# Performance work log

Measured on AMD Instinct MI355X. Metric: run time of the kernel, lower is better.

The kernel has to match this reference:

```python
import jax, jax.numpy as jnp
import numpy as np
from jax import lax

RADIUS = 3
ITERATION = 6
KSIZE = 2 * RADIUS + 1


def _make_kernels(r):
    # Build the 8 directional side-window box kernels, order: L,R,U,D,NW,NE,SW,SE
    k = 2 * r + 1
    f = np.ones((k, k), np.float32)
    L = f.copy(); L[:, r + 1:] = 0
    R = f.copy(); R[:, :r] = 0
    U = f.copy(); U[r + 1:, :] = 0
    D = f.copy(); D[:r, :] = 0
    NW = U.copy(); NW[:, r + 1:] = 0
    NE = U.copy(); NE[:, :r] = 0
    SW = D.copy(); SW[:, r + 1:] = 0
    SE = D.copy(); SE[:, :r] = 0
    n_half = (r + 1) * k          # normalizer for half windows
    n_quarter = (r + 1) ** 2      # normalizer for quarter windows
    ks = np.stack([L / n_half, R / n_half, U / n_half, D / n_half,
                   NW / n_quarter, NE / n_quarter, SW / n_quarter, SE / n_quarter])
    return jnp.asarray(ks[:, None, :, :])  # (8,1,k,k) OIHW


def setup_inputs() -> dict:
    key = jax.random.key(0)
    k1, k2 = jax.random.split(key)
    im = jax.random.normal(k1, (4, 3, 512, 512), dtype=jnp.float32)
    pert = jax.random.normal(k2, (4, 3, 512, 512), dtype=jnp.float32)
    return {"im": im, "pert": pert}


def reference(im, pert):
    b, c, h, w = im.shape
    W = _make_kernels(RADIUS)

    def conv8(x):  # (N,1,h,w) -> (N,8,h,w), SAME padding of radius
        return lax.conv_general_dilated(
            x, W, window_strides=(1, 1),
            padding=[(RADIUS, RADIUS), (RADIUS, RADIUS)],
            dimension_numbers=("NCHW", "OIHW", "NCHW"))

    # channels are processed independently with identical kernels -> fold c into batch
    im_f = im.reshape(b * c, 1, h, w)
    pert_f = pert.reshape(b * c, 1, h, w)

    def step(carry, _):
        im_ch, pert_ch = carry
        z = jnp.concatenate([im_ch, pert_ch], axis=0)  # (2N,1,h,w)
        dz = conv8(z) - z                              # (2N,8,h,w), broadcast over dir
        d, dd = jnp.split(dz, 2, axis=0)
        idx = jnp.argmin(jnp.abs(d), axis=1, keepdims=True)    # (N,1,h,w)
        dm = jnp.take_along_axis(d, idx, axis=1)
        ddm = jnp.take_along_axis(dd, idx, axis=1)
        return (im_ch + dm, pert_ch + ddm), None

    (im_f, pert_f), _ = lax.scan(step, (im_f, pert_f), None, length=ITERATION)
    # torch code overwrites every channel of res with pert_ch -> result is filtered pert
    return pert_f.reshape(b, c, h, w)
```

## Files before the change

### kernel.cpp

```cpp
#include <hip/hip_runtime.h>

#define HH 512
#define WW 512
#define NIMG 12
#define RAD 3
#define TW 64
#define TH 32
#define LW (TW + 2*RAD)
#define LH (TH + 2*RAD)
#define RPW 8

typedef float v2 __attribute__((ext_vector_type(2)));

#define GPTR const __attribute__((address_space(1))) void*
#define LPTR __attribute__((address_space(3))) void*

template <int NR, int LDW, class F>
__device__ __forceinline__ void ring_pass(
    const float* __restrict__ SI, const float* __restrict__ SP,
    int r0, int tx, F emit)
{
    const float w28 = 1.0f / 28.0f;
    const float w16 = 0.0625f;
    const v2 w28v = {w28, w28};
    const v2 w16v = {w16, w16};

    v2    pi[7][4];
    v2    hlr[7];
    float cc[7];

    auto rowload = [&](int slot, int m) {
        const float* rI = SI + m * LDW + tx;
        float w0 = rI[0], w1 = rI[1], w2 = rI[2], w3 = rI[3],
              w4 = rI[4], w5 = rI[5], w6 = rI[6];
        pi[slot][0] = (v2){w0, w3};
        pi[slot][1] = (v2){w1, w4};
        pi[slot][2] = (v2){w2, w5};
        pi[slot][3] = (v2){w3, w6};
        const float* rP = SP + m * LDW + tx;
        float b0 = rP[0], b1 = rP[1], b2 = rP[2], b3 = rP[3],
              b4 = rP[4], b5 = rP[5], b6 = rP[6];
        hlr[slot] = (v2){(b0 + b1) + (b2 + b3), (b3 + b4) + (b5 + b6)};
        cc[slot] = b3;
    };

    #pragma unroll
    for (int m = 0; m < 7; ++m)
        rowload(m, r0 + m);

    #pragma unroll
    for (int jj = 0; jj < NR; ++jj) {
        v2 aLR = {0.f, 0.f}, aQN = {0.f, 0.f}, aQS = {0.f, 0.f};
        #pragma unroll
        for (int dy = 0; dy < 7; ++dy) {
            const int s = (jj + dy) % 7;
            #pragma unroll
            for (int dx = 0; dx < 4; ++dx)
                aLR = __builtin_elementwise_fma(pi[s][dx], w28v, aLR);
        }
        float U = 0.f, Dd = 0.f;
        #pragma unroll
        for (int dy = 0; dy < 4; ++dy) {
            const int su = (jj + dy) % 7;
            const int sd = (jj + dy + 3) % 7;
            U = fmaf(pi[su][0].x, w28, U);  U = fmaf(pi[su][1].x, w28, U);
            U = fmaf(pi[su][2].x, w28, U);  U = fmaf(pi[su][3].x, w28, U);
            U = fmaf(pi[su][1].y, w28, U);  U = fmaf(pi[su][2].y, w28, U);
            U = fmaf(pi[su][3].y, w28, U);
            Dd = fmaf(pi[sd][0].x, w28, Dd); Dd = fmaf(pi[sd][1].x, w28, Dd);
            Dd = fmaf(pi[sd][2].x, w28, Dd); Dd = fmaf(pi[sd][3].x, w28, Dd);
            Dd = fmaf(pi[sd][1].y, w28, Dd); Dd = fmaf(pi[sd][2].y, w28, Dd);
            Dd = fmaf(pi[sd][3].y, w28, Dd);
            #pragma unroll
            for (int dx = 0; dx < 4; ++dx) {
                aQN = __builtin_elementwise_fma(pi[su][dx], w16v, aQN);
                aQS = __builtin_elementwise_fma(pi[sd][dx], w16v, aQS);
            }
        }

        const float cI = pi[(jj + 3) % 7][3].x;
        const v2 cI2 = {cI, cI};
        const v2 d01 = aLR - cI2;
        const float d2 = U - cI, d3 = Dd - cI;
        const v2 d45 = aQN - cI2;
        const v2 d67 = aQS - cI2;
        float d[8] = {d01.x, d01.y, d2, d3, d45.x, d45.y, d67.x, d67.y};

        float e[8];
        const int p0 = (jj + 0) % 7, p1 = (jj + 1) % 7, p2 = (jj + 2) % 7,
                  p3 = (jj + 3) % 7, p4 = (jj + 4) % 7, p5 = (jj + 5) % 7,
                  p6 = (jj + 6) % 7;
        const float cP = cc[p3];
        {
            v2 qN = ((hlr[p0] + hlr[p1]) + (hlr[p2] + hlr[p3]));
            v2 qS = ((hlr[p3] + hlr[p4]) + (hlr[p5] + hlr[p6]));
            float cu = ((cc[p0] + cc[p1]) + (cc[p2] + cc[p3]));
            float cd = ((cc[p3] + cc[p4]) + (cc[p5] + cc[p6]));
            const v2 cP2 = {cP, cP};
            v2 eLR = (qN + qS - hlr[p3]) * w28v - cP2;
            v2 eQN = qN * w16v - cP2;
            v2 eQS = qS * w16v - cP2;
            e[0] = eLR.x;  e[1] = eLR.y;
            e[2] = (qN.x + qN.y - cu) * w28 - cP;
            e[3] = (qS.x + qS.y - cd) * w28 - cP;
            e[4] = eQN.x;  e[5] = eQN.y;
            e[6] = eQS.x;  e[7] = eQS.y;
        }

        float bestAbs = fabsf(d[0]);
        float bd = d[0];
        float be = e[0];
        #pragma unroll
        for (int j = 1; j < 8; ++j) {
            float a = fabsf(d[j]);
            bool take = a < bestAbs;
            bestAbs = take ? a : bestAbs;
            bd = take ? d[j] : bd;
            be = take ? e[j] : be;
        }

        emit(jj, cI + bd, cP + be);

        if (jj < NR - 1)
            rowload(jj % 7, r0 + jj + 7);
    }
}

__global__ __launch_bounds__(256) void swf_step(
    const float* __restrict__ im_in, const float* __restrict__ pe_in,
    float* __restrict__ im_out, float* __restrict__ pe_out, int storeIm)
{
    __shared__ float sI[LH * LW];
    __shared__ float sP[LH * LW];

    const int tid = threadIdx.x;
    const int tx = tid & 63;
    const int wv = tid >> 6;
    const int x0 = blockIdx.x * TW;
    const int y0 = blockIdx.y * TH;
    const size_t base = (size_t)blockIdx.z * (size_t)(HH * WW);
    const float* imb = im_in + base;
    const float* peb = pe_in + base;

    const bool interior = (blockIdx.x >= 1) && (blockIdx.x <= 6) &&
                          (blockIdx.y >= 1) && (blockIdx.y <= (HH/TH - 2));
    if (interior) {
        #pragma unroll 1
        for (int r = wv; r < LH; r += 4) {
            const float* gI = imb + (size_t)(y0 - RAD + r) * WW + (x0 - RAD);
            const float* gP = peb + (size_t)(y0 - RAD + r) * WW + (x0 - RAD);
            __builtin_amdgcn_global_load_lds((GPTR)(gI + tx),
                                             (LPTR)(&sI[r * LW]), 4, 0, 0);
            __builtin_amdgcn_global_load_lds((GPTR)(gP + tx),
                                             (LPTR)(&sP[r * LW]), 4, 0, 0);
            if (tx < 6) {
                __builtin_amdgcn_global_load_lds((GPTR)(gI + 64 + tx),
                                                 (LPTR)(&sI[r * LW + 64]), 4, 0, 0);
                __builtin_amdgcn_global_load_lds((GPTR)(gP + 64 + tx),
                                                 (LPTR)(&sP[r * LW + 64]), 4, 0, 0);
            }
        }
    } else {
        for (int i = tid; i < LH * LW; i += 256) {
            int r = i / LW;
            int c = i - r * LW;
            int gy = y0 - RAD + r;
            int gx = x0 - RAD + c;
            bool ok = ((unsigned)gy < (unsigned)HH) && ((unsigned)gx < (unsigned)WW);
            int gi = gy * WW + gx;
            sI[i] = ok ? imb[gi] : 0.0f;
            sP[i] = ok ? peb[gi] : 0.0f;
        }
    }
    __syncthreads();

    const int r0 = wv * RPW;
    ring_pass<RPW, LW>(&sI[0], &sP[0], r0, tx,
        [&](int jj, float vI, float vP) {
            const size_t gi = base + (size_t)(y0 + r0 + jj) * WW + (x0 + tx);
            if (storeIm) im_out[gi] = vI;
            pe_out[gi] = vP;
        });
}

extern "C" void kernel_launch(void* const* d_in, const int* in_sizes, int n_in,
                              void* d_out, int out_size, void* d_ws, size_t ws_size,
                              hipStream_t stream) {
    const float* im0 = (const float*)d_in[0];
    const float* pe0 = (const float*)d_in[1];
    float* out = (float*)d_out;

    const size_t npix = (size_t)NIMG * HH * WW;
    float* imA = (float*)d_ws;
    float* imB = imA + npix;
    float* peA = imB + npix;
    float* peB = out;

    dim3 grid(WW / TW, HH / TH, NIMG);
    dim3 block(256);

    swf_step<<<grid, block, 0, stream>>>(im0, pe0, imA, peA, 1);
    swf_step<<<grid, block, 0, stream>>>(imA, peA, imB, peB, 1);
    swf_step<<<grid, block, 0, stream>>>(imB, peB, imA, peA, 1);
    swf_step<<<grid, block, 0, stream>>>(imA, peA, imB, peB, 1);
    swf_step<<<grid, block, 0, stream>>>(imB, peB, imA, peA, 1);
    swf_step<<<grid, block, 0, stream>>>(imA, peA, imB, out, 0);
}
```

Before: 207.9 us.

## Give each wavefront a private LDS slab and drop the block barrier

Each wavefront now loads its own 14-row halo slab into a private LDS region instead of sharing one 38-row tile across the block. The __syncthreads is replaced by a per-wave vmcnt wait, so waves no longer stall on each other. The cost is redundant loads, since halo rows are fetched twice by adjacent waves (14 rows per 8 output rows instead of 38 per 32), which raises LDS usage and global/L2 traffic. It also depends on the vmcnt wait being sufficient for global_load_lds completion within a wave.

```diff
diff --git a/kernel.cpp b/kernel.cpp
--- a/kernel.cpp
+++ b/kernel.cpp
@@ -7,8 +7,8 @@
 #define TW 64
 #define TH 32
 #define LW (TW + 2*RAD)
-#define LH (TH + 2*RAD)
 #define RPW 8
+#define SLABR (RPW + 6)
 
 typedef float v2 __attribute__((ext_vector_type(2)));
 
@@ -130,54 +130,65 @@
     const float* __restrict__ im_in, const float* __restrict__ pe_in,
     float* __restrict__ im_out, float* __restrict__ pe_out, int storeIm)
 {
-    __shared__ float sI[LH * LW];
-    __shared__ float sP[LH * LW];
+    __shared__ float sI[4][SLABR * LW];
+    __shared__ float sP[4][SLABR * LW];
 
     const int tid = threadIdx.x;
     const int tx = tid & 63;
     const int wv = tid >> 6;
     const int x0 = blockIdx.x * TW;
-    const int y0 = blockIdx.y * TH;
+    const int yw = blockIdx.y * TH + wv * RPW;
     const size_t base = (size_t)blockIdx.z * (size_t)(HH * WW);
     const float* imb = im_in + base;
     const float* peb = pe_in + base;
 
-    const bool interior = (blockIdx.x >= 1) && (blockIdx.x <= 6) &&
-                          (blockIdx.y >= 1) && (blockIdx.y <= (HH/TH - 2));
-    if (interior) {
+    float* slabI = &sI[wv][0];
+    float* slabP = &sP[wv][0];
+
+    const bool wInterior = (blockIdx.x >= 1) && (blockIdx.x <= 6) &&
+                           (yw - RAD >= 0) && (yw + RPW + 2 < HH);
+    if (wInterior) {
         #pragma unroll 1
-        for (int r = wv; r < LH; r += 4) {
-            const float* gI = imb + (size_t)(y0 - RAD + r) * WW + (x0 - RAD);
-            const float* gP = peb + (size_t)(y0 - RAD + r) * WW + (x0 - RAD);
+        for (int r = 0; r < SLABR; ++r) {
+            const float* gI = imb + (size_t)(yw - RAD + r) * WW + (x0 - RAD);
+            const float* gP = peb + (size_t)(yw - RAD + r) * WW + (x0 - RAD);
             __builtin_amdgcn_global_load_lds((GPTR)(gI + tx),
-                                             (LPTR)(&sI[r * LW]), 4, 0, 0);
+                                             (LPTR)(&slabI[r * LW]), 4, 0, 0);
             __builtin_amdgcn_global_load_lds((GPTR)(gP + tx),
-                                             (LPTR)(&sP[r * LW]), 4, 0, 0);
+                                             (LPTR)(&slabP[r * LW]), 4, 0, 0);
             if (tx < 6) {
                 __builtin_amdgcn_global_load_lds((GPTR)(gI + 64 + tx),
-                                                 (LPTR)(&sI[r * LW + 64]), 4, 0, 0);
+                                                 (LPTR)(&slabI[r * LW + 64]), 4, 0, 0);
                 __builtin_amdgcn_global_load_lds((GPTR)(gP + 64 + tx),
-                                                 (LPTR)(&sP[r * LW + 64]), 4, 0, 0);
+                                                 (LPTR)(&slabP[r * LW + 64]), 4, 0, 0);
             }
         }
     } else {
-        for (int i = tid; i < LH * LW; i += 256) {
-            int r = i / LW;
-            int c = i - r * LW;
-            int gy = y0 - RAD + r;
-            int gx = x0 - RAD + c;
-            bool ok = ((unsigned)gy < (unsigned)HH) && ((unsigned)gx < (unsigned)WW);
-            int gi = gy * WW + gx;
-            sI[i] = ok ? imb[gi] : 0.0f;
-            sP[i] = ok ? peb[gi] : 0.0f;
+        #pragma unroll 1
+        for (int r = 0; r < SLABR; ++r) {
+            const int gy = yw - RAD + r;
+            const bool oky = (unsigned)gy < (unsigned)HH;
+            {
+                const int gx = x0 - RAD + tx;
+                const bool ok = oky && ((unsigned)gx < (unsigned)WW);
+                const int gi = gy * WW + gx;
+                slabI[r * LW + tx] = ok ? imb[gi] : 0.0f;
+                slabP[r * LW + tx] = ok ? peb[gi] : 0.0f;
+            }
+            if (tx < 6) {
+                const int gx = x0 - RAD + 64 + tx;
+                const bool ok = oky && ((unsigned)gx < (unsigned)WW);
+                const int gi = gy * WW + gx;
+                slabI[r * LW + 64 + tx] = ok ? imb[gi] : 0.0f;
+                slabP[r * LW + 64 + tx] = ok ? peb[gi] : 0.0f;
+            }
         }
     }
-    __syncthreads();
-
-    const int r0 = wv * RPW;
-    ring_pass<RPW, LW>(&sI[0], &sP[0], r0, tx,
+    asm volatile("s_waitcnt vmcnt(0)" ::: "memory");
+
+    ring_pass<RPW, LW>(slabI, slabP, 0, tx,
         [&](int jj, float vI, float vP) {
-            const size_t gi = base + (size_t)(y0 + r0 + jj) * WW + (x0 + tx);
+            const size_t gi = base + (size_t)(yw + jj) * WW + (x0 + tx);
             if (storeIm) im_out[gi] = vI;
             pe_out[gi] = vP;
         });
```

Result: slower. 323.3 us (+55.5%).
